# Performance work log

Measured on AMD Instinct MI355X. Metric: run time of the kernel, lower is better.

## Reference

```python
import jax, jax.numpy as jnp
import numpy as np

# Dims. NOTE: TransmorpherLayer2d passes (dim_head, num_heads) positionally into an
# attention class whose signature is (num_heads, dim_head) -> attention runs with
# H = dim_head = 64 heads of size Dh = num_heads = 12. embed_dim D = 768 either way.
B, S, L = 1, 64, 512
H, Dh = 64, 12
D = H * Dh          # 768
DFF = 3072
EPS = 1e-5


def _ln(x, g, b):
    m = x.mean(-1, keepdims=True)
    v = ((x - m) ** 2).mean(-1, keepdims=True)
    return (x - m) / jnp.sqrt(v + EPS) * g + b


def setup_inputs() -> dict:
    key = jax.random.key(0)
    ks = jax.random.split(key, 6)
    sd = 0.02
    p = {
        'x': jax.random.normal(ks[0], (B, S, L, D), jnp.float32),
        'w_row': jax.random.normal(ks[1], (D, 3 * D), jnp.float32) * sd,
        'b_row': jnp.zeros((3 * D,), jnp.float32),
        'w_col': jax.random.normal(ks[2], (D, 3 * D), jnp.float32) * sd,
        'b_col': jnp.zeros((3 * D,), jnp.float32),
        'g_a1': jnp.ones((D,), jnp.float32), 'be_a1': jnp.zeros((D,), jnp.float32),
        'g_a2': jnp.ones((D,), jnp.float32), 'be_a2': jnp.zeros((D,), jnp.float32),
        'w1': jax.random.normal(ks[3], (D, DFF), jnp.float32) * sd,
        'b1f': jnp.zeros((DFF,), jnp.float32),
        'w2': jax.random.normal(ks[4], (DFF, D), jnp.float32) * sd,
        'b2f': jnp.zeros((D,), jnp.float32),
        'g_n1': jnp.ones((D,), jnp.float32), 'be_n1': jnp.zeros((D,), jnp.float32),
        'g_n2': jnp.ones((D,), jnp.float32), 'be_n2': jnp.zeros((D,), jnp.float32),
    }
    return p


def reference(x, w_row, b_row, w_col, b_col, g_a1, be_a1, g_a2, be_a2,
              w1, b1f, w2, b2f, g_n1, be_n1, g_n2, be_n2):
    def qkv(t, w, b):
        q, k, v = jnp.split(t @ w + b, 3, axis=-1)
        rs = lambda a: a.reshape(B, S, L, H, Dh)
        return rs(q), rs(k), rs(v)

    # ---- TiedAxialSelfAttention2d (no 1/sqrt(d) scaling, tied over S) ----
    q, k, v = qkv(x, w_row, b_row)
    row_attn = jax.nn.softmax(jnp.einsum('bsihc,bsjhc->bhij', q, k), axis=-1)  # [B,H,L,L]
    row_out = jnp.einsum('bhij,bsjhd->bsihd', row_attn, v).reshape(B, S, L, D)
    out = _ln(x + row_out, g_a1, be_a1)

    q, k, v = qkv(out, w_col, b_col)
    col_attn = jax.nn.softmax(jnp.einsum('bilhc,bjlhc->bhijl', q, k), axis=-2)  # [B,H,S,S,L]
    col_out = jnp.einsum('bhijl,bjlhd->bilhd', col_attn, v).reshape(B, S, L, D)
    out = _ln(out + col_out, g_a2, be_a2)

    # ---- TransmorpherLayer2d residual + FFN (post-LN) ----
    y = _ln(x + out, g_n1, be_n1)
    ff = jax.nn.relu(y @ w1 + b1f) @ w2 + b2f
    return _ln(y + ff, g_n2, be_n2)
```

## Files before the change

### kernel.cpp

```cpp
#include <hip/hip_runtime.h>

typedef unsigned short u16;
typedef unsigned int u32;
typedef __attribute__((ext_vector_type(8))) short short8;
typedef __attribute__((ext_vector_type(4))) float floatx4;

#define LN_EPS 1e-5f
#define REG 6291456L

__device__ __forceinline__ float b2f(u16 u) {
    return __builtin_bit_cast(float, (u32)u << 16);
}
__device__ __forceinline__ u16 f2b(float f) {
    u32 x = __builtin_bit_cast(u32, f);
    return (u16)((x + 0x7fffu + ((x >> 16) & 1u)) >> 16);
}

__device__ __forceinline__ void gload16(const u16* g, u16* l) {
    __builtin_amdgcn_global_load_lds(
        (const __attribute__((address_space(1))) void*)g,
        (__attribute__((address_space(3))) void*)l, 16, 0, 0);
}

template<int BN_, int EPI, int RELU, int HASBIAS, int SMAJ>
__global__ __launch_bounds__(256, 2) void gemm_dma(
    const u16* __restrict__ A, const u16* __restrict__ BT,
    const float* __restrict__ bias, void* __restrict__ C,
    int Nb, int K, long sA, long sB, long sC, int colbase)
{
    constexpr int NCH = (128 + BN_) / 64;
    constexpr int JF  = BN_ / 32;
    __shared__ u16 lds[(128 + BN_) * 32];

    const u16* Az = A + (long)blockIdx.z * sA;
    const u16* Bz = BT + (long)blockIdx.z * sB;
    const int n0 = blockIdx.x * BN_;
    const int tid = threadIdx.x;
    const int lane = tid & 63;
    const int wm = ((tid >> 6) >> 1) * 64;
    const int wn = ((tid >> 6) & 1) * (BN_ / 2);
    const int lrow = lane & 15;
    const int quad = lane >> 4;

    floatx4 acc[4][JF];
#pragma unroll
    for (int i = 0; i < 4; i++)
#pragma unroll
        for (int j = 0; j < JF; j++)
            acc[i][j] = (floatx4){0.f, 0.f, 0.f, 0.f};

    for (int kt = 0; kt < K; kt += 32) {
#pragma unroll
        for (int it = 0; it < NCH; it++) {
            const int idx = tid + it * 256;
            const u16* src;
            if (idx < 512) {
                const int row = idx >> 2;
                const int ch  = (idx & 3) * 8;
                const long grow = SMAJ
                    ? ((long)(row >> 1) * 512 + (blockIdx.y << 1) + (row & 1))
                    : ((long)blockIdx.y * 128 + row);
                src = Az + grow * K + kt + ch;
            } else {
                const int bidx = idx - 512;
                const int row = bidx >> 2;
                const int ch  = (bidx & 3) * 8;
                src = Bz + (long)(n0 + row) * K + kt + ch;
            }
            gload16(src, &lds[idx * 8]);
        }
        __syncthreads();

        short8 af[4], bfr[JF];
#pragma unroll
        for (int i = 0; i < 4; i++)
            af[i] = *(const short8*)&lds[(wm + i * 16 + lrow) * 32 + quad * 8];
#pragma unroll
        for (int j = 0; j < JF; j++)
            bfr[j] = *(const short8*)&lds[4096 + (wn + j * 16 + lrow) * 32 + quad * 8];
#pragma unroll
        for (int i = 0; i < 4; i++)
#pragma unroll
            for (int j = 0; j < JF; j++)
                acc[i][j] = __builtin_amdgcn_mfma_f32_16x16x32_bf16(
                    af[i], bfr[j], acc[i][j], 0, 0, 0);
        __syncthreads();
    }

    const int z = blockIdx.z;
#pragma unroll
    for (int j = 0; j < JF; j++) {
        const int n = n0 + wn + j * 16 + lrow;
        int t = 0, jj = n;
        if (EPI == 8 || EPI == 9) { t = n / 192; jj = n - t * 192; }
        const int hl = jj / 12;
        const int cc = jj - hl * 12;
        float bv = 0.f;
        if (HASBIAS)
            bv = (EPI == 8 || EPI == 9) ? bias[t * 768 + colbase + jj]
                                        : bias[colbase + n];
#pragma unroll
        for (int i = 0; i < 4; i++) {
            const int mb = wm + i * 16 + quad * 4;
#pragma unroll
            for (int r = 0; r < 4; r++) {
                const int ml = mb + r;
                float v = acc[i][j][r] + bv;
                if (RELU) v = fmaxf(v, 0.f);
                if (EPI == 0) {
                    const long m = (long)blockIdx.y * 128 + ml;
                    ((u16*)C)[m * Nb + n] = f2b(v);
                } else if (EPI == 1) {
                    const long m = (long)blockIdx.y * 128 + ml;
                    ((float*)C)[(long)z * sC + m * Nb + n] = v;
                } else if (EPI == 3) {
                    const int gm = blockIdx.y * 128 + ml;
                    const int s = gm >> 9, iL = gm & 511;
                    ((u16*)C)[(long)hl * 393216 + (long)(s * 12 + cc) * 512 + iL] = f2b(v);
                } else if (EPI == 4) {
                    const int m = blockIdx.y * 128 + ml;
                    ((u16*)C)[((long)hl * 512 + m) * 768 + colbase + z * 12 + cc] = f2b(v);
                } else if (EPI == 8) {
                    const int s = ml >> 1, iL = (blockIdx.y << 1) + (ml & 1);
                    ((u16*)C)[(long)t * REG + ((long)hl * 512 + iL) * 768 + s * 12 + cc] = f2b(v);
                } else if (EPI == 9) {
                    const int s = ml >> 1, l = (blockIdx.y << 1) + (ml & 1);
                    ((u16*)C)[(long)t * REG + (long)hl * 393216 + (long)l * 768 + s * 12 + cc] = f2b(v);
                }
            }
        }
    }
}

__global__ __launch_bounds__(256) void cast_kernel(
    const float* __restrict__ X, u16* __restrict__ Xb)
{
    const long i = ((long)blockIdx.x * 256 + threadIdx.x) * 8;
    float4 a = *(const float4*)(X + i);
    float4 b = *(const float4*)(X + i + 4);
    u16 t8[8] = { f2b(a.x), f2b(a.y), f2b(a.z), f2b(a.w),
                  f2b(b.x), f2b(b.y), f2b(b.z), f2b(b.w) };
    *(uint4*)(Xb + i) = *(const uint4*)t8;
}

__global__ __launch_bounds__(256) void transpose_kernel(
    const float* __restrict__ In, u16* __restrict__ Out, int R, int Ccols)
{
    __shared__ u16 tile[32][33];
    int tx = threadIdx.x & 31;
    int ty = threadIdx.x >> 5;
    int c0 = blockIdx.x * 32;
    int r0 = blockIdx.y * 32;
#pragma unroll
    for (int rr = 0; rr < 32; rr += 8)
        tile[ty + rr][tx] = f2b(In[(long)(r0 + ty + rr) * Ccols + c0 + tx]);
    __syncthreads();
#pragma unroll
    for (int rr = 0; rr < 32; rr += 8)
        Out[(long)(c0 + ty + rr) * R + r0 + tx] = tile[tx][ty + rr];
}

__global__ __launch_bounds__(256) void pack_qk_kernel(
    const float* __restrict__ In, u16* __restrict__ Out)
{
    __shared__ u16 tile[32][33];
    int tx = threadIdx.x & 31;
    int ty = threadIdx.x >> 5;
    int p0 = blockIdx.x * 32;
    int k0 = blockIdx.y * 32;
    int hg = p0 / 384, rem = p0 % 384;
    int t = rem / 192, j0 = rem % 192;
    int c0 = t * 768 + hg * 192 + j0;
#pragma unroll
    for (int rr = 0; rr < 32; rr += 8)
        tile[ty + rr][tx] = f2b(In[(long)(k0 + ty + rr) * 2304 + c0 + tx]);
    __syncthreads();
#pragma unroll
    for (int rr = 0; rr < 32; rr += 8)
        Out[(long)(p0 + ty + rr) * 768 + k0 + tx] = tile[tx][ty + rr];
}

__global__ __launch_bounds__(256) void pack_v_kernel(
    const float* __restrict__ In, u16* __restrict__ Out)
{
    __shared__ u16 tile[32][33];
    int tx = threadIdx.x & 31;
    int ty = threadIdx.x >> 5;
    int p0 = blockIdx.x * 32;
    int k0 = blockIdx.y * 32;
    int hg = p0 / 192, j0 = p0 % 192;
    int c0 = 1536 + hg * 192 + j0;
#pragma unroll
    for (int rr = 0; rr < 32; rr += 8)
        tile[ty + rr][tx] = f2b(In[(long)(k0 + ty + rr) * 2304 + c0 + tx]);
    __syncthreads();
#pragma unroll
    for (int rr = 0; rr < 32; rr += 8)
        Out[(long)(p0 + ty + rr) * 768 + k0 + tx] = tile[tx][ty + rr];
}

__global__ __launch_bounds__(256) void qkv_pack_kernel(
    const float* __restrict__ In, u16* __restrict__ Out)
{
    __shared__ u16 tile[32][33];
    int tx = threadIdx.x & 31;
    int ty = threadIdx.x >> 5;
    int p0 = blockIdx.x * 32;
    int k0 = blockIdx.y * 32;
    int hg = p0 / 576, r0 = p0 % 576;
    int t = r0 / 192, j0 = r0 % 192;
    int c0 = t * 768 + hg * 192 + j0;
#pragma unroll
    for (int rr = 0; rr < 32; rr += 8)
        tile[ty + rr][tx] = f2b(In[(long)(k0 + ty + rr) * 2304 + c0 + tx]);
    __syncthreads();
#pragma unroll
    for (int rr = 0; rr < 32; rr += 8)
        Out[(long)(p0 + ty + rr) * 768 + k0 + tx] = tile[tx][ty + rr];
}

__global__ __launch_bounds__(256) void softmax_kernel(
    const float* __restrict__ S, u16* __restrict__ P)
{
    const long r = blockIdx.x;
    const float* sp = S + r * 512;
    int t = threadIdx.x;
    float a = sp[t], b = sp[t + 256];
    __shared__ float red[256];
    red[t] = fmaxf(a, b);
    __syncthreads();
    for (int o = 128; o > 0; o >>= 1) {
        if (t < o) red[t] = fmaxf(red[t], red[t + o]);
        __syncthreads();
    }
    float mx = red[0];
    __syncthreads();
    float ea = __expf(a - mx), eb = __expf(b - mx);
    red[t] = ea + eb;
    __syncthreads();
    for (int o = 128; o > 0; o >>= 1) {
        if (t < o) red[t] += red[t + o];
        __syncthreads();
    }
    float inv = 1.0f / red[0];
    P[r * 512 + t] = f2b(ea * inv);
    P[r * 512 + t + 256] = f2b(eb * inv);
}

template<int AF, int BF, int OF>
__global__ __launch_bounds__(256) void ln_add_kernel(
    const void* __restrict__ Xa, const void* __restrict__ Xb,
    const float* __restrict__ g, const float* __restrict__ be,
    void* __restrict__ Out)
{
    const long r = blockIdx.x;
    int t = threadIdx.x;
    float v[3]; float sm = 0.f, s2 = 0.f;
#pragma unroll
    for (int e = 0; e < 3; e++) {
        long c = r * 768 + t + e * 256;
        float xa = AF ? ((const float*)Xa)[c] : b2f(((const u16*)Xa)[c]);
        float xb = BF ? ((const float*)Xb)[c] : b2f(((const u16*)Xb)[c]);
        float x = xa + xb;
        v[e] = x; sm += x; s2 += x * x;
    }
    __shared__ float r1[256], r2[256];
    r1[t] = sm; r2[t] = s2;
    __syncthreads();
    for (int o = 128; o > 0; o >>= 1) {
        if (t < o) { r1[t] += r1[t + o]; r2[t] += r2[t + o]; }
        __syncthreads();
    }
    float mean = r1[0] * (1.0f / 768.0f);
    float var  = r2[0] * (1.0f / 768.0f) - mean * mean;
    float rstd = rsqrtf(var + LN_EPS);
#pragma unroll
    for (int e = 0; e < 3; e++) {
        int c = t + e * 256;
        float o = (v[e] - mean) * rstd * g[c] + be[c];
        if (OF) ((float*)Out)[r * 768 + c] = o;
        else    ((u16*)Out)[r * 768 + c] = f2b(o);
    }
}

__global__ __launch_bounds__(256) void ln_ln_kernel(
    const u16* __restrict__ A, const u16* __restrict__ B,
    const float* __restrict__ X,
    const float* __restrict__ g1, const float* __restrict__ be1,
    const float* __restrict__ g2, const float* __restrict__ be2,
    float* __restrict__ Out, u16* __restrict__ Outb)
{
    const long r = blockIdx.x;
    int t = threadIdx.x;
    __shared__ float r1[256], r2[256];

    float u[3]; float sm = 0.f, s2 = 0.f;
#pragma unroll
    for (int e = 0; e < 3; e++) {
        long c = r * 768 + t + e * 256;
        float x = b2f(A[c]) + b2f(B[c]);
        u[e] = x; sm += x; s2 += x * x;
    }
    r1[t] = sm; r2[t] = s2;
    __syncthreads();
    for (int o = 128; o > 0; o >>= 1) {
        if (t < o) { r1[t] += r1[t + o]; r2[t] += r2[t + o]; }
        __syncthreads();
    }
    float mean1 = r1[0] * (1.0f / 768.0f);
    float var1  = r2[0] * (1.0f / 768.0f) - mean1 * mean1;
    float rstd1 = rsqrtf(var1 + LN_EPS);
    __syncthreads();

    float w[3]; sm = 0.f; s2 = 0.f;
#pragma unroll
    for (int e = 0; e < 3; e++) {
        int c = t + e * 256;
        float tv = (u[e] - mean1) * rstd1 * g1[c] + be1[c];
        float wv = X[r * 768 + c] + tv;
        w[e] = wv; sm += wv; s2 += wv * wv;
    }
    r1[t] = sm; r2[t] = s2;
    __syncthreads();
    for (int o = 128; o > 0; o >>= 1) {
        if (t < o) { r1[t] += r1[t + o]; r2[t] += r2[t + o]; }
        __syncthreads();
    }
    float mean2 = r1[0] * (1.0f / 768.0f);
    float var2  = r2[0] * (1.0f / 768.0f) - mean2 * mean2;
    float rstd2 = rsqrtf(var2 + LN_EPS);
#pragma unroll
    for (int e = 0; e < 3; e++) {
        int c = t + e * 256;
        float o = (w[e] - mean2) * rstd2 * g2[c] + be2[c];
        Out[r * 768 + c] = o;
        Outb[r * 768 + c] = f2b(o);
    }
}

__global__ __launch_bounds__(64) void col_attn_kernel(
    const u16* __restrict__ qc, const u16* __restrict__ kc,
    const u16* __restrict__ vc, u16* __restrict__ Out, int hbase)
{
    const int hh = blockIdx.x >> 9;
    const int l  = blockIdx.x & 511;
    const int i  = threadIdx.x;
    const long base = ((long)hh * 512 + l) * 768;
    __shared__ float Ks[64][12];
    __shared__ float Vs[64][12];
    float q[12];
#pragma unroll
    for (int c = 0; c < 12; c++) {
        q[c] = b2f(qc[base + i * 12 + c]);
        Ks[i][c] = b2f(kc[base + i * 12 + c]);
        Vs[i][c] = b2f(vc[base + i * 12 + c]);
    }
    __syncthreads();
    float sc[64];
#pragma unroll
    for (int j = 0; j < 64; j++) {
        float a = 0.f;
#pragma unroll
        for (int c = 0; c < 12; c++) a += q[c] * Ks[j][c];
        sc[j] = a;
    }
    float m = sc[0];
#pragma unroll
    for (int j = 1; j < 64; j++) m = fmaxf(m, sc[j]);
    float sum = 0.f;
#pragma unroll
    for (int j = 0; j < 64; j++) { sc[j] = __expf(sc[j] - m); sum += sc[j]; }
    float inv = 1.0f / sum;
    float o[12];
#pragma unroll
    for (int c = 0; c < 12; c++) o[c] = 0.f;
#pragma unroll
    for (int j = 0; j < 64; j++) {
        float p = sc[j] * inv;
#pragma unroll
        for (int c = 0; c < 12; c++) o[c] += p * Vs[j][c];
    }
    u16* op = Out + ((long)i * 512 + l) * 768 + hbase + hh * 12;
#pragma unroll
    for (int c = 0; c < 12; c++) op[c] = f2b(o[c]);
}

extern "C" void kernel_launch(void* const* d_in, const int* in_sizes, int n_in,
                              void* d_out, int out_size, void* d_ws, size_t ws_size,
                              hipStream_t stream)
{
    (void)in_sizes; (void)n_in; (void)out_size; (void)ws_size;

    const float* x     = (const float*)d_in[0];
    const float* w_row = (const float*)d_in[1];
    const float* b_row = (const float*)d_in[2];
    const float* w_col = (const float*)d_in[3];
    const float* b_col = (const float*)d_in[4];
    const float* g_a1  = (const float*)d_in[5];
    const float* be_a1 = (const float*)d_in[6];
    const float* g_a2  = (const float*)d_in[7];
    const float* be_a2 = (const float*)d_in[8];
    const float* w1    = (const float*)d_in[9];
    const float* b1f   = (const float*)d_in[10];
    const float* w2    = (const float*)d_in[11];
    const float* b2f_  = (const float*)d_in[12];
    const float* g_n1  = (const float*)d_in[13];
    const float* be_n1 = (const float*)d_in[14];
    const float* g_n2  = (const float*)d_in[15];
    const float* be_n2 = (const float*)d_in[16];
    float* outp = (float*)d_out;

    char* wp = (char*)d_ws;
    auto alloc = [&](size_t bytes) -> void* {
        void* p = (void*)wp;
        wp += (bytes + 255) & ~(size_t)255;
        return p;
    };
    u16*   wPqk   = (u16*)alloc((size_t)1536 * 768 * 2);
    u16*   wPv    = (u16*)alloc((size_t)768 * 768 * 2);
    u16*   wPcol  = (u16*)alloc((size_t)2304 * 768 * 2);
    u16*   w1T    = (u16*)alloc((size_t)3072 * 768 * 2);
    u16*   w2T    = (u16*)alloc((size_t)768 * 3072 * 2);
    u16*   bufA   = (u16*)alloc((size_t)32768 * 768 * 2);
    u16*   bufB   = (u16*)alloc((size_t)32768 * 768 * 2);
    u16*   qkvg   = (u16*)alloc((size_t)3 * 16 * 512 * 768 * 2);
    float* scores = (float*)alloc((size_t)16 * 512 * 512 * 4);
    u16*   probs  = (u16*)alloc((size_t)16 * 512 * 512 * 2);
    u16*   hidden = qkvg;
    u16*   xb     = bufB;
    u16*   ybf    = bufB;
    float* y      = outp;

    pack_qk_kernel<<<dim3(48, 24), 256, 0, stream>>>(w_row, wPqk);
    pack_v_kernel<<<dim3(24, 24), 256, 0, stream>>>(w_row, wPv);
    qkv_pack_kernel<<<dim3(72, 24), 256, 0, stream>>>(w_col, wPcol);
    transpose_kernel<<<dim3(96, 24), 256, 0, stream>>>(w1, w1T, 768, 3072);
    transpose_kernel<<<dim3(24, 96), 256, 0, stream>>>(w2, w2T, 3072, 768);
    cast_kernel<<<12288, 256, 0, stream>>>(x, xb);

    for (int hg = 0; hg < 4; hg++) {
        gemm_dma<192, 8, 0, 1, 1><<<dim3(2, 256), 256, 0, stream>>>(
            xb, wPqk + (long)hg * 384 * 768, b_row, qkvg,
            384, 768, 0, 0, 0, hg * 192);
        gemm_dma<192, 3, 0, 1, 0><<<dim3(1, 256), 256, 0, stream>>>(
            xb, wPv + (long)hg * 192 * 768, b_row, qkvg + 2 * REG,
            192, 768, 0, 0, 0, 1536 + hg * 192);
        gemm_dma<128, 1, 0, 0, 0><<<dim3(4, 4, 16), 256, 0, stream>>>(
            qkvg, qkvg + REG, nullptr, scores,
            512, 768, (long)512 * 768, (long)512 * 768, (long)512 * 512, 0);
        softmax_kernel<<<8192, 256, 0, stream>>>(scores, probs);
        gemm_dma<128, 4, 0, 0, 0><<<dim3(6, 4, 16), 256, 0, stream>>>(
            probs, qkvg + 2 * REG, nullptr, bufA,
            768, 512, (long)512 * 512, (long)768 * 512, 0, hg * 192);
    }
    ln_add_kernel<1, 0, 0><<<32768, 256, 0, stream>>>(x, bufA, g_a1, be_a1, bufB);

    for (int hg = 0; hg < 4; hg++) {
        gemm_dma<192, 9, 0, 1, 1><<<dim3(3, 256), 256, 0, stream>>>(
            bufB, wPcol + (long)hg * 576 * 768, b_col, qkvg,
            576, 768, 0, 0, 0, hg * 192);
        col_attn_kernel<<<8192, 64, 0, stream>>>(
            qkvg, qkvg + REG, qkvg + 2 * REG, bufA, hg * 192);
    }
    ln_ln_kernel<<<32768, 256, 0, stream>>>(
        bufB, bufA, x, g_a2, be_a2, g_n1, be_n1, y, ybf);

    for (int mc = 0; mc < 4; mc++) {
        const long off = (long)mc * 8192 * 768;
        gemm_dma<192, 0, 1, 1, 0><<<dim3(16, 64), 256, 0, stream>>>(
            ybf + off, w1T, b1f, hidden, 3072, 768, 0, 0, 0, 0);
        gemm_dma<192, 0, 0, 1, 0><<<dim3(4, 64), 256, 0, stream>>>(
            hidden, w2T, b2f_, bufA + off, 768, 3072, 0, 0, 0, 0);
    }
    ln_add_kernel<1, 0, 1><<<32768, 256, 0, stream>>>(y, bufA, g_n2, be_n2, outp);
}
```

Baseline: 1.786 ms.

## Double-buffer GEMM LDS tiles with DMA prefetch and XOR-swizzled layout

Doubles the shared-memory tile buffer so the global-to-LDS DMA loads for the next K-slice are issued before the MFMA work on the current slice, overlapping memory latency with compute and removing one barrier per iteration. It also applies an XOR swizzle to the 16-byte chunk position within each row to reduce LDS bank conflicts on fragment reads. Source and destination offsets are precomputed outside the loop. This doubles LDS usage per block, which may affect occupancy at two blocks per CU, and relies on manual waitcnt and barrier ordering for correctness.

Result: faster. 1.577 ms (-11.7%).

```diff
diff --git a/kernel.cpp b/kernel.cpp
--- a/kernel.cpp
+++ b/kernel.cpp
@@ -28,9 +28,10 @@
     const float* __restrict__ bias, void* __restrict__ C,
     int Nb, int K, long sA, long sB, long sC, int colbase)
 {
-    constexpr int NCH = (128 + BN_) / 64;
-    constexpr int JF  = BN_ / 32;
-    __shared__ u16 lds[(128 + BN_) * 32];
+    constexpr int NCH  = (128 + BN_) / 64;
+    constexpr int JF   = BN_ / 32;
+    constexpr int TILE = (128 + BN_) * 32;
+    __shared__ u16 lds[2 * TILE];
 
     const u16* Az = A + (long)blockIdx.z * sA;
     const u16* Bz = BT + (long)blockIdx.z * sB;
@@ -49,42 +50,76 @@
         for (int j = 0; j < JF; j++)
             acc[i][j] = (floatx4){0.f, 0.f, 0.f, 0.f};
 
+    const u16* sbase[NCH];
+    int doff[NCH];
+#pragma unroll
+    for (int it = 0; it < NCH; it++) {
+        const int idx = tid + it * 256;
+        const int slot = idx & 3;
+        doff[it] = idx * 8;
+        if (idx < 512) {
+            const int row = idx >> 2;
+            const int ch  = (slot ^ ((row >> 1) & 3)) * 8;
+            const long grow = SMAJ
+                ? ((long)(row >> 1) * 512 + (blockIdx.y << 1) + (row & 1))
+                : ((long)blockIdx.y * 128 + row);
+            sbase[it] = Az + grow * K + ch;
+        } else {
+            const int row = (idx - 512) >> 2;
+            const int ch  = (slot ^ ((row >> 1) & 3)) * 8;
+            sbase[it] = Bz + (long)(n0 + row) * K + ch;
+        }
+    }
+
+    int aoff[4], boff[JF];
+#pragma unroll
+    for (int i = 0; i < 4; i++) {
+        const int r = wm + i * 16 + lrow;
+        aoff[i] = r * 32 + ((quad ^ ((r >> 1) & 3)) * 8);
+    }
+#pragma unroll
+    for (int j = 0; j < JF; j++) {
+        const int r = wn + j * 16 + lrow;
+        boff[j] = 4096 + r * 32 + ((quad ^ ((r >> 1) & 3)) * 8);
+    }
+
+#pragma unroll
+    for (int it = 0; it < NCH; it++)
+        gload16(sbase[it], &lds[doff[it]]);
+    asm volatile("s_waitcnt vmcnt(0)" ::: "memory");
+    __builtin_amdgcn_s_barrier();
+    __builtin_amdgcn_sched_barrier(0);
+
+    int cb = 0;
     for (int kt = 0; kt < K; kt += 32) {
-#pragma unroll
-        for (int it = 0; it < NCH; it++) {
-            const int idx = tid + it * 256;
-            const u16* src;
-            if (idx < 512) {
-                const int row = idx >> 2;
-                const int ch  = (idx & 3) * 8;
-                const long grow = SMAJ
-                    ? ((long)(row >> 1) * 512 + (blockIdx.y << 1) + (row & 1))
-                    : ((long)blockIdx.y * 128 + row);
-                src = Az + grow * K + kt + ch;
-            } else {
-                const int bidx = idx - 512;
-                const int row = bidx >> 2;
-                const int ch  = (bidx & 3) * 8;
-                src = Bz + (long)(n0 + row) * K + kt + ch;
-            }
-            gload16(src, &lds[idx * 8]);
+        if (kt + 32 < K) {
+            const int nb = (cb ^ 1) * TILE;
+#pragma unroll
+            for (int it = 0; it < NCH; it++)
+                gload16(sbase[it] + kt + 32, &lds[nb + doff[it]]);
         }
-        __syncthreads();
-
+        __builtin_amdgcn_sched_barrier(0);
+
+        const int b0 = cb * TILE;
         short8 af[4], bfr[JF];
 #pragma unroll
         for (int i = 0; i < 4; i++)
-            af[i] = *(const short8*)&lds[(wm + i * 16 + lrow) * 32 + quad * 8];
+            af[i] = *(const short8*)&lds[b0 + aoff[i]];
 #pragma unroll
         for (int j = 0; j < JF; j++)
-            bfr[j] = *(const short8*)&lds[4096 + (wn + j * 16 + lrow) * 32 + quad * 8];
+            bfr[j] = *(const short8*)&lds[b0 + boff[j]];
 #pragma unroll
         for (int i = 0; i < 4; i++)
 #pragma unroll
             for (int j = 0; j < JF; j++)
                 acc[i][j] = __builtin_amdgcn_mfma_f32_16x16x32_bf16(
                     af[i], bfr[j], acc[i][j], 0, 0, 0);
-        __syncthreads();
+
+        __builtin_amdgcn_sched_barrier(0);
+        asm volatile("s_waitcnt vmcnt(0)" ::: "memory");
+        __builtin_amdgcn_s_barrier();
+        __builtin_amdgcn_sched_barrier(0);
+        cb ^= 1;
     }
 
     const int z = blockIdx.z;
```
